# Performance work log

Hardware: AMD Instinct MI355X
Metric: run time of the kernel (lower is better)

## Reference

```python
import jax, jax.numpy as jnp
import numpy as np

N_NODES = 40962
N_EDGES = 245760
K = 10  # gaussian kernels
D = 2   # pseudo-coordinate dim
EPS = 1e-15


def gmm_conv(x, edge_index, pseudo, g, mu, sigma, root, bias):
    """PyG GMMConv with aggr='mean', root_weight=True.
    x: [N, Cin], edge_index: [2, E] (row 0 = source j, row 1 = target i),
    pseudo: [E, D], g: [Cin, K*Cout], mu/sigma: [K, D], root: [Cin, Cout], bias: [Cout].
    """
    src, dst = edge_index[0], edge_index[1]
    E = pseudo.shape[0]
    # Gaussian mixture edge weights: [E, K]
    diff = pseudo[:, None, :] - mu[None, :, :]                     # [E, K, D]
    w = jnp.exp(jnp.sum(-0.5 * diff * diff / (EPS + sigma[None] ** 2), axis=-1))
    xj = x[src]                                                    # [E, Cin] gather
    y = (xj @ g).reshape(E, K, -1)                                 # [E, K, Cout]
    msg = jnp.sum(y * w[:, :, None], axis=1)                       # [E, Cout]
    agg = jax.ops.segment_sum(msg, dst, num_segments=N_NODES)      # scatter-add
    deg = jax.ops.segment_sum(jnp.ones((E,), x.dtype), dst, num_segments=N_NODES)
    agg = agg / jnp.maximum(deg, 1.0)[:, None]                     # mean aggregation
    return agg + x @ root + bias


def setup_inputs() -> dict:
    key = jax.random.key(0)
    ks = jax.random.split(key, 20)
    Cin, Ch, Cout = 64, 64, 128
    sc = lambda fan: 1.0 / np.sqrt(fan)
    inp = {
        "x": jax.random.normal(ks[0], (N_NODES, Cin), jnp.float32),
        "edge_index": jax.random.randint(ks[1], (2, N_EDGES), 0, N_NODES, jnp.int32),
        "pseudo": jax.random.uniform(ks[2], (N_EDGES, D), jnp.float32),
        # conv1: Cin -> Ch
        "g1": jax.random.normal(ks[3], (Cin, K * Ch), jnp.float32) * sc(Cin),
        "mu1": jax.random.uniform(ks[4], (K, D), jnp.float32),
        "sigma1": jax.random.uniform(ks[5], (K, D), jnp.float32) + 0.5,
        "root1": jax.random.normal(ks[6], (Cin, Ch), jnp.float32) * sc(Cin),
        "b1": jnp.zeros((Ch,), jnp.float32),
        # conv2: Ch -> Cout
        "g2": jax.random.normal(ks[7], (Ch, K * Cout), jnp.float32) * sc(Ch),
        "mu2": jax.random.uniform(ks[8], (K, D), jnp.float32),
        "sigma2": jax.random.uniform(ks[9], (K, D), jnp.float32) + 0.5,
        "root2": jax.random.normal(ks[10], (Ch, Cout), jnp.float32) * sc(Ch),
        "b2": jnp.zeros((Cout,), jnp.float32),
        # shortcut: Cin -> Cout (size_in != size_out)
        "gs": jax.random.normal(ks[11], (Cin, K * Cout), jnp.float32) * sc(Cin),
        "mus": jax.random.uniform(ks[12], (K, D), jnp.float32),
        "sigmas": jax.random.uniform(ks[13], (K, D), jnp.float32) + 0.5,
        "roots": jax.random.normal(ks[14], (Cin, Cout), jnp.float32) * sc(Cin),
        "bs": jnp.zeros((Cout,), jnp.float32),
    }
    return inp


def reference(x, edge_index, pseudo, g1, mu1, sigma1, root1, b1,
              g2, mu2, sigma2, root2, b2, gs, mus, sigmas, roots, bs):
    h = gmm_conv(x, edge_index, pseudo, g1, mu1, sigma1, root1, b1)
    h = jax.nn.relu(h)
    y = gmm_conv(h, edge_index, pseudo, g2, mu2, sigma2, root2, b2)
    x_s = gmm_conv(x, edge_index, pseudo, gs, mus, sigmas, roots, bs)
    return jax.nn.relu(y + x_s)
```

## Files before the change

kernel.cpp:

```cpp
#include <hip/hip_runtime.h>
#include <hip/hip_bf16.h>

using bf16 = __hip_bfloat16;
typedef __attribute__((ext_vector_type(8))) short short8;
typedef __attribute__((ext_vector_type(4))) float float4v;

#define N_NODES 40962
#define N_EDGES 245760
#define NP      41024
#define KG      10
#define SCAN_B  256
#define NBLK    ((NP + SCAN_B - 1) / SCAN_B)
#define GRIDF   (NP / 16)

#define CVT_V   (N_NODES * 64 / 8)
#define CVT_BLK ((CVT_V + 255) / 256)
#define W3_BLK  (N_EDGES / 256)
#define PACK_N  (64 * 704 + 2 * 128 * 704)
#define PACK_BLK (PACK_N / 256)

#define ZRS  680
#define ZT   10880

__device__ __forceinline__ float ldf(const void* p, size_t i, int isf32) {
    return isf32 ? ((const float*)p)[i] : __bfloat162float(((const bf16*)p)[i]);
}
__device__ __forceinline__ float blo(unsigned u) { return __uint_as_float(u << 16); }
__device__ __forceinline__ float bhi(unsigned u) { return __uint_as_float(u & 0xffff0000u); }
__device__ __forceinline__ unsigned pk2(float a, float b) {
    union { bf16 h[2]; unsigned u; } t;
    t.h[0] = __float2bfloat16(a);
    t.h[1] = __float2bfloat16(b);
    return t.u;
}
__device__ __forceinline__ int rfl(int v) { return __builtin_amdgcn_readfirstlane(v); }

__global__ void k_detect_count(const void* x, const int* __restrict__ ei,
                               int* __restrict__ flag, int* __restrict__ deg) {
    if (blockIdx.x == 0) {
        __shared__ int huge_c, zero_even;
        if (threadIdx.x == 0) { huge_c = 0; zero_even = 0; }
        __syncthreads();
        const bf16* xb = (const bf16*)x;
        int lh = 0, lz = 0;
        for (int i = threadIdx.x; i < 8192; i += 256) {
            float v = __bfloat162float(xb[i]);
            if (!(fabsf(v) <= 1e4f)) lh++;
            if ((i & 1) == 0 && v == 0.0f) lz++;
        }
        atomicAdd(&huge_c, lh);
        atomicAdd(&zero_even, lz);
        __syncthreads();
        if (threadIdx.x == 0) flag[0] = (huge_c > 0 || zero_even > 3000) ? 1 : 0;
    } else {
        int e = (blockIdx.x - 1) * 256 + threadIdx.x;
        if (e < N_EDGES) atomicAdd(&deg[ei[N_EDGES + e]], 1);
    }
}

__global__ void k_scan1(const int* __restrict__ deg, int* __restrict__ offs,
                        int* __restrict__ bsum) {
    __shared__ int buf[SCAN_B];
    int t = threadIdx.x, b = blockIdx.x;
    int i = b * SCAN_B + t;
    int v = (i < NP) ? deg[i] : 0;
    buf[t] = v;
    __syncthreads();
    for (int off = 1; off < SCAN_B; off <<= 1) {
        int a = (t >= off) ? buf[t - off] : 0;
        __syncthreads();
        buf[t] += a;
        __syncthreads();
    }
    if (i < NP) offs[i] = buf[t] - v;
    if (t == SCAN_B - 1) bsum[b] = buf[t];
}

__global__ void k_scan3m(int* __restrict__ offs, const int* __restrict__ bsum,
                         const int* __restrict__ deg, int* __restrict__ cur,
                         float* __restrict__ invdeg) {
    __shared__ int buf[256];
    int t = threadIdx.x, b = blockIdx.x;
    int v = (t < NBLK) ? bsum[t] : 0;
    buf[t] = v;
    __syncthreads();
    for (int off = 1; off < 256; off <<= 1) {
        int a = (t >= off) ? buf[t - off] : 0;
        __syncthreads();
        buf[t] += a;
        __syncthreads();
    }
    int bofs = (b > 0) ? buf[b - 1] : 0;
    int total = buf[NBLK - 1];
    int i = b * 256 + t;
    if (i < NP) {
        int o = offs[i] + bofs;
        offs[i] = o;
        cur[i] = o;
        int d = deg[i];
        invdeg[i] = 1.0f / (float)(d > 1 ? d : 1);
    }
    if (i == 0) offs[NP] = total;
}

__global__ void k_fill(const int* __restrict__ ei, int* __restrict__ cur,
                       int* __restrict__ ep, int* __restrict__ csr_src) {
    int e = blockIdx.x * 256 + threadIdx.x;
    if (e < N_EDGES) {
        int pos = atomicAdd(&cur[ei[N_EDGES + e]], 1);
        ep[e] = pos;
        csr_src[pos] = ei[e];
    }
}

__device__ __forceinline__ void gw_one(float p0, float p1, const void* mu,
                                       const void* sg, int f, float* out) {
#pragma unroll
    for (int k = 0; k < KG; k++) {
        float m0 = ldf(mu, 2 * k + 0, f), m1 = ldf(mu, 2 * k + 1, f);
        float s0 = ldf(sg, 2 * k + 0, f), s1 = ldf(sg, 2 * k + 1, f);
        float d0 = p0 - m0, d1 = p1 - m1;
        float t = -0.5f * (d0 * d0 / (1e-15f + s0 * s0) + d1 * d1 / (1e-15f + s1 * s1));
        out[k] = __expf(t);
    }
}

__device__ __forceinline__ void pack_frag(const void* g, const void* root, int f,
                                          int idx, int Cout, bf16* Bp) {
    int j = idx & 7;
    int lane = (idx >> 3) & 63;
    int rem = idx >> 9;
    int kc = rem % 22;
    int n = rem / 22;
    int col = n * 16 + (lane & 15);
    int k = kc * 32 + (lane >> 4) * 8 + j;
    float v;
    if (k < 512) {
        int cin = k >> 3, kg = k & 7;
        v = ldf(g, (size_t)cin * (KG * Cout) + (size_t)kg * Cout + col, f);
    } else if (k < 640) {
        int jj = k - 512;
        int cin = jj >> 1, kg = 8 + (jj & 1);
        v = ldf(g, (size_t)cin * (KG * Cout) + (size_t)kg * Cout + col, f);
    } else {
        v = ldf(root, (size_t)(k - 640) * Cout + col, f);
    }
    Bp[idx] = __float2bfloat16(v);
}

__global__ void k_prep_all(const void* __restrict__ x, const void* __restrict__ pseudo,
                           const void* mu1, const void* sg1, const void* mu2,
                           const void* sg2, const void* mus, const void* sgs,
                           const void* g1, const void* root1, const void* g2,
                           const void* root2, const void* gs, const void* roots,
                           const int* __restrict__ flag, const int* __restrict__ ep,
                           bf16* __restrict__ Xf, bf16* __restrict__ wcab,
                           bf16* __restrict__ wc2, bf16* wt1p, bf16* wt2p,
                           bf16* wtsp) {
    int b = blockIdx.x;
    int tid = threadIdx.x;
    int f = flag[0];
    if (b < CVT_BLK) {
        int i = b * 256 + tid;
        if (i < CVT_V) {
            int node = i >> 3, j = i & 7;
            uint4 u;
            if (f) {
                const float4* xf = (const float4*)x;
                float4 a = xf[2 * i], c = xf[2 * i + 1];
                union { bf16 t[8]; uint4 u; } tt;
                tt.t[0] = __float2bfloat16(a.x); tt.t[1] = __float2bfloat16(a.y);
                tt.t[2] = __float2bfloat16(a.z); tt.t[3] = __float2bfloat16(a.w);
                tt.t[4] = __float2bfloat16(c.x); tt.t[5] = __float2bfloat16(c.y);
                tt.t[6] = __float2bfloat16(c.z); tt.t[7] = __float2bfloat16(c.w);
                u = tt.u;
            } else {
                u = ((const uint4*)x)[i];
            }
            *(uint4*)(Xf + (size_t)node * 64 + j * 8) = u;
        }
    } else if (b < CVT_BLK + W3_BLK) {
        int e = (b - CVT_BLK) * 256 + tid;
        float p0 = ldf(pseudo, (size_t)e * 2 + 0, f);
        float p1 = ldf(pseudo, (size_t)e * 2 + 1, f);
        float o1[KG], o2[KG], os[KG];
        gw_one(p0, p1, mu1, sg1, f, o1);
        gw_one(p0, p1, mu2, sg2, f, o2);
        gw_one(p0, p1, mus, sgs, f, os);
        int pos = ep[e];
        unsigned* d = (unsigned*)wcab + (size_t)pos * 10;
        d[0] = pk2(o1[0], o1[1]); d[1] = pk2(o1[2], o1[3]);
        d[2] = pk2(o1[4], o1[5]); d[3] = pk2(o1[6], o1[7]);
        d[4] = pk2(o1[8], o1[9]);
        d[5] = pk2(os[0], os[1]); d[6] = pk2(os[2], os[3]);
        d[7] = pk2(os[4], os[5]); d[8] = pk2(os[6], os[7]);
        d[9] = pk2(os[8], os[9]);
        unsigned* d2 = (unsigned*)wc2 + (size_t)pos * 5;
        d2[0] = pk2(o2[0], o2[1]); d2[1] = pk2(o2[2], o2[3]);
        d2[2] = pk2(o2[4], o2[5]); d2[3] = pk2(o2[6], o2[7]);
        d2[4] = pk2(o2[8], o2[9]);
    } else {
        int idx = (b - CVT_BLK - W3_BLK) * 256 + tid;
        if (idx < 64 * 704) {
            pack_frag(g1, root1, f, idx, 64, wt1p);
        } else if (idx < 64 * 704 + 128 * 704) {
            pack_frag(g2, root2, f, idx - 64 * 704, 128, wt2p);
        } else {
            pack_frag(gs, roots, f, idx - 64 * 704 - 128 * 704, 128, wtsp);
        }
    }
}

__device__ __forceinline__ float ldxf(const bf16* X, int src, int lane) {
    return __bfloat162float(X[(size_t)src * 64 + lane]);
}

__device__ __forceinline__ int clampe(int idx) {
    return idx > N_EDGES - 1 ? N_EDGES - 1 : idx;
}

__device__ __forceinline__ void store_zlds(bf16* z, int r, int lane, const float* a,
                                           float inv) {
    union { bf16 h[8]; uint4 u; } p;
#pragma unroll
    for (int k = 0; k < 8; k++) p.h[k] = __float2bfloat16(a[k] * inv);
    *(uint4*)(z + r * ZRS + lane * 8) = p.u;
    *(unsigned*)(z + r * ZRS + 512 + lane * 2) = pk2(a[8] * inv, a[9] * inv);
}

__device__ __forceinline__ void gather_dual(const int* __restrict__ offs,
                                            const int* __restrict__ csr_src,
                                            const unsigned* __restrict__ wb,
                                            const bf16* __restrict__ X, int node,
                                            int lane, float* aa, float* ab) {
#pragma unroll
    for (int k = 0; k < KG; k++) { aa[k] = 0.0f; ab[k] = 0.0f; }
    int beg = rfl(offs[node]);
    int end = rfl(offs[node + 1]);
    int cnt = end - beg;
    int s4 = rfl(csr_src[clampe(beg + 4)]);
    float xv0 = ldxf(X, rfl(csr_src[clampe(beg + 0)]), lane);
    float xv1 = ldxf(X, rfl(csr_src[clampe(beg + 1)]), lane);
    float xv2 = ldxf(X, rfl(csr_src[clampe(beg + 2)]), lane);
    float xv3 = ldxf(X, rfl(csr_src[clampe(beg + 3)]), lane);
    const unsigned* wp0 = wb + (size_t)clampe(beg + 0) * 10;
    unsigned c0 = wp0[0], c1 = wp0[1], c2 = wp0[2], c3 = wp0[3], c4 = wp0[4];
    unsigned c5 = wp0[5], c6 = wp0[6], c7 = wp0[7], c8 = wp0[8], c9 = wp0[9];
    const unsigned* wp1 = wb + (size_t)clampe(beg + 1) * 10;
    unsigned n0 = wp1[0], n1 = wp1[1], n2 = wp1[2], n3 = wp1[3], n4 = wp1[4];
    unsigned n5 = wp1[5], n6 = wp1[6], n7 = wp1[7], n8 = wp1[8], n9 = wp1[9];
    for (int t = 0; t < cnt; ++t) {
        int s5 = rfl(csr_src[clampe(beg + t + 5)]);
        float xv4 = ldxf(X, s4, lane);
        const unsigned* wp2 = wb + (size_t)clampe(beg + t + 2) * 10;
        unsigned m0 = wp2[0], m1 = wp2[1], m2 = wp2[2], m3 = wp2[3], m4 = wp2[4];
        unsigned m5 = wp2[5], m6 = wp2[6], m7 = wp2[7], m8 = wp2[8], m9 = wp2[9];
        aa[0] += blo(c0) * xv0; aa[1] += bhi(c0) * xv0;
        aa[2] += blo(c1) * xv0; aa[3] += bhi(c1) * xv0;
        aa[4] += blo(c2) * xv0; aa[5] += bhi(c2) * xv0;
        aa[6] += blo(c3) * xv0; aa[7] += bhi(c3) * xv0;
        aa[8] += blo(c4) * xv0; aa[9] += bhi(c4) * xv0;
        ab[0] += blo(c5) * xv0; ab[1] += bhi(c5) * xv0;
        ab[2] += blo(c6) * xv0; ab[3] += bhi(c6) * xv0;
        ab[4] += blo(c7) * xv0; ab[5] += bhi(c7) * xv0;
        ab[6] += blo(c8) * xv0; ab[7] += bhi(c8) * xv0;
        ab[8] += blo(c9) * xv0; ab[9] += bhi(c9) * xv0;
        xv0 = xv1; xv1 = xv2; xv2 = xv3; xv3 = xv4; s4 = s5;
        c0 = n0; c1 = n1; c2 = n2; c3 = n3; c4 = n4;
        c5 = n5; c6 = n6; c7 = n7; c8 = n8; c9 = n9;
        n0 = m0; n1 = m1; n2 = m2; n3 = m3; n4 = m4;
        n5 = m5; n6 = m6; n7 = m7; n8 = m8; n9 = m9;
    }
}

__device__ __forceinline__ void gather_one(const int* __restrict__ offs,
                                           const int* __restrict__ csr_src,
                                           const unsigned* __restrict__ wb,
                                           const bf16* __restrict__ X, int node,
                                           int lane, float* acc) {
#pragma unroll
    for (int k = 0; k < KG; k++) acc[k] = 0.0f;
    int beg = rfl(offs[node]);
    int end = rfl(offs[node + 1]);
    int cnt = end - beg;
    int s4 = rfl(csr_src[clampe(beg + 4)]);
    float xv0 = ldxf(X, rfl(csr_src[clampe(beg + 0)]), lane);
    float xv1 = ldxf(X, rfl(csr_src[clampe(beg + 1)]), lane);
    float xv2 = ldxf(X, rfl(csr_src[clampe(beg + 2)]), lane);
    float xv3 = ldxf(X, rfl(csr_src[clampe(beg + 3)]), lane);
    const unsigned* wp0 = wb + (size_t)clampe(beg + 0) * 5;
    unsigned c0 = wp0[0], c1 = wp0[1], c2 = wp0[2], c3 = wp0[3], c4 = wp0[4];
    const unsigned* wp1 = wb + (size_t)clampe(beg + 1) * 5;
    unsigned n0 = wp1[0], n1 = wp1[1], n2 = wp1[2], n3 = wp1[3], n4 = wp1[4];
    for (int t = 0; t < cnt; ++t) {
        int s5 = rfl(csr_src[clampe(beg + t + 5)]);
        float xv4 = ldxf(X, s4, lane);
        const unsigned* wp2 = wb + (size_t)clampe(beg + t + 2) * 5;
        unsigned m0 = wp2[0], m1 = wp2[1], m2 = wp2[2], m3 = wp2[3], m4 = wp2[4];
        acc[0] += blo(c0) * xv0; acc[1] += bhi(c0) * xv0;
        acc[2] += blo(c1) * xv0; acc[3] += bhi(c1) * xv0;
        acc[4] += blo(c2) * xv0; acc[5] += bhi(c2) * xv0;
        acc[6] += blo(c3) * xv0; acc[7] += bhi(c3) * xv0;
        acc[8] += blo(c4) * xv0; acc[9] += bhi(c4) * xv0;
        xv0 = xv1; xv1 = xv2; xv2 = xv3; xv3 = xv4; s4 = s5;
        c0 = n0; c1 = n1; c2 = n2; c3 = n3; c4 = n4;
        n0 = m0; n1 = m1; n2 = m2; n3 = m3; n4 = m4;
    }
}

__global__ __launch_bounds__(512) void k_fusedA(
    const int* __restrict__ offs, const int* __restrict__ csr_src,
    const bf16* __restrict__ wcab, const float* __restrict__ invdeg,
    const bf16* __restrict__ Xf, const bf16* __restrict__ wt1p,
    const bf16* __restrict__ wtsp, const void* __restrict__ b1,
    const void* __restrict__ bs, const int* __restrict__ flag,
    bf16* __restrict__ hf, bf16* __restrict__ ys) {
    __shared__ bf16 z1[ZT];
    __shared__ bf16 zs[ZT];
    int lane = threadIdx.x & 63;
    int wave = threadIdx.x >> 6;
    int bid = blockIdx.x;

#pragma unroll
    for (int i = 0; i < 2; i++) {
        int r = wave * 2 + i;
        int node = bid * 16 + r;
        float aa[KG], ab[KG];
        gather_dual(offs, csr_src, (const unsigned*)wcab, Xf, node, lane, aa, ab);
        float inv = invdeg[node];
        store_zlds(z1, r, lane, aa, inv);
        store_zlds(zs, r, lane, ab, inv);
    }
    __syncthreads();

    int m = lane & 15, quad = lane >> 4;
    int row0 = bid * 16;
    int f = flag[0];

    {
        float4v acc4 = (float4v){0.f, 0.f, 0.f, 0.f};
        const bf16* brow = wtsp + ((size_t)(wave * 22) * 64 + lane) * 8;
        const bf16* xrow = Xf + (size_t)(row0 + m) * 64;
#pragma unroll
        for (int kc = 0; kc < 22; kc++) {
            short8 a = (kc < 20)
                ? *(const short8*)(zs + m * ZRS + kc * 32 + quad * 8)
                : *(const short8*)(xrow + (kc - 20) * 32 + quad * 8);
            short8 b = *(const short8*)(brow + (size_t)kc * 512);
            acc4 = __builtin_amdgcn_mfma_f32_16x16x32_bf16(a, b, acc4, 0, 0, 0);
        }
        int gcol = wave * 16 + m;
        float bv = ldf(bs, gcol, f);
#pragma unroll
        for (int r = 0; r < 4; r++) {
            int grow = row0 + quad * 4 + r;
            if (grow >= N_NODES) continue;
            ys[(size_t)grow * 128 + gcol] = __float2bfloat16(acc4[r] + bv);
        }
    }

    if (wave < 4) {
        float4v acc4 = (float4v){0.f, 0.f, 0.f, 0.f};
        const bf16* brow = wt1p + ((size_t)(wave * 22) * 64 + lane) * 8;
        const bf16* xrow = Xf + (size_t)(row0 + m) * 64;
#pragma unroll
        for (int kc = 0; kc < 22; kc++) {
            short8 a = (kc < 20)
                ? *(const short8*)(z1 + m * ZRS + kc * 32 + quad * 8)
                : *(const short8*)(xrow + (kc - 20) * 32 + quad * 8);
            short8 b = *(const short8*)(brow + (size_t)kc * 512);
            acc4 = __builtin_amdgcn_mfma_f32_16x16x32_bf16(a, b, acc4, 0, 0, 0);
        }
        int gcol = wave * 16 + m;
        float bv = ldf(b1, gcol, f);
#pragma unroll
        for (int r = 0; r < 4; r++) {
            int grow = row0 + quad * 4 + r;
            if (grow >= N_NODES) continue;
            float v = fmaxf(acc4[r] + bv, 0.f);
            hf[(size_t)grow * 64 + gcol] = __float2bfloat16(v);
        }
    }
}

__global__ __launch_bounds__(512) void k_fusedB(
    const int* __restrict__ offs, const int* __restrict__ csr_src,
    const bf16* __restrict__ wc2, const float* __restrict__ invdeg,
    const bf16* __restrict__ hf, const bf16* __restrict__ wt2p,
    const void* __restrict__ b2, const bf16* __restrict__ ys,
    const int* __restrict__ flag, void* __restrict__ out) {
    __shared__ bf16 z[ZT];
    int lane = threadIdx.x & 63;
    int wave = threadIdx.x >> 6;
    int bid = blockIdx.x;

#pragma unroll
    for (int i = 0; i < 2; i++) {
        int r = wave * 2 + i;
        int node = bid * 16 + r;
        float acc[KG];
        gather_one(offs, csr_src, (const unsigned*)wc2, hf, node, lane, acc);
        store_zlds(z, r, lane, acc, invdeg[node]);
    }
    __syncthreads();

    int m = lane & 15, quad = lane >> 4;
    int row0 = bid * 16;
    int f = flag[0];
    float4v acc4 = (float4v){0.f, 0.f, 0.f, 0.f};
    const bf16* brow = wt2p + ((size_t)(wave * 22) * 64 + lane) * 8;
    const bf16* hrow = hf + (size_t)(row0 + m) * 64;
#pragma unroll
    for (int kc = 0; kc < 22; kc++) {
        short8 a = (kc < 20)
            ? *(const short8*)(z + m * ZRS + kc * 32 + quad * 8)
            : *(const short8*)(hrow + (kc - 20) * 32 + quad * 8);
        short8 b = *(const short8*)(brow + (size_t)kc * 512);
        acc4 = __builtin_amdgcn_mfma_f32_16x16x32_bf16(a, b, acc4, 0, 0, 0);
    }
    int gcol = wave * 16 + m;
    float bv = ldf(b2, gcol, f);
#pragma unroll
    for (int r = 0; r < 4; r++) {
        int grow = row0 + quad * 4 + r;
        if (grow >= N_NODES) continue;
        size_t oidx = (size_t)grow * 128 + gcol;
        float v = fmaxf(acc4[r] + bv + __bfloat162float(ys[oidx]), 0.f);
        if (f) ((float*)out)[oidx] = v;
        else   ((bf16*)out)[oidx] = __float2bfloat16(v);
    }
}

extern "C" void kernel_launch(void* const* d_in, const int* in_sizes, int n_in,
                              void* d_out, int out_size, void* d_ws, size_t ws_size,
                              hipStream_t stream) {
    const void* x      = d_in[0];
    const int*  ei     = (const int*)d_in[1];
    const void* pseudo = d_in[2];
    const void* g1     = d_in[3];
    const void* mu1    = d_in[4];
    const void* sg1    = d_in[5];
    const void* root1  = d_in[6];
    const void* b1     = d_in[7];
    const void* g2     = d_in[8];
    const void* mu2    = d_in[9];
    const void* sg2    = d_in[10];
    const void* root2  = d_in[11];
    const void* b2     = d_in[12];
    const void* gs     = d_in[13];
    const void* mus    = d_in[14];
    const void* sgs    = d_in[15];
    const void* roots  = d_in[16];
    const void* bs     = d_in[17];

    char* ws = (char*)d_ws;
    size_t off = 0;
    auto alloc = [&](size_t bytes) -> char* {
        char* p = ws + off;
        off += (bytes + 255) & ~(size_t)255;
        return p;
    };
    const size_t XFS = (size_t)NP * 64 * 2;

    int*   flag   = (int*)alloc(256);
    int*   deg    = (int*)alloc((size_t)NP * 4);
    int*   offs   = (int*)alloc((size_t)(NP + 1) * 4);
    int*   cur    = (int*)alloc((size_t)NP * 4);
    float* invdeg = (float*)alloc((size_t)NP * 4);
    int*   bsum   = (int*)alloc((size_t)NBLK * 4);
    int*   ep     = (int*)alloc((size_t)N_EDGES * 4);
    int*   csrs   = (int*)alloc((size_t)N_EDGES * 4);
    bf16*  Xf     = (bf16*)alloc(XFS);
    bf16*  hf     = (bf16*)alloc(XFS);
    bf16*  ys     = (bf16*)alloc((size_t)NP * 128 * 2);
    bf16*  wt1p   = (bf16*)alloc((size_t)64 * 704 * 2);
    bf16*  wt2p   = (bf16*)alloc((size_t)128 * 704 * 2);
    bf16*  wtsp   = (bf16*)alloc((size_t)128 * 704 * 2);
    bf16*  wcab   = (bf16*)alloc((size_t)N_EDGES * 20 * 2);
    bf16*  wc2    = (bf16*)alloc((size_t)N_EDGES * 10 * 2);
    (void)ws_size;

    hipMemsetAsync(deg, 0, (size_t)NP * 4, stream);
    k_detect_count<<<1 + (N_EDGES + 255) / 256, 256, 0, stream>>>(x, ei, flag, deg);
    k_scan1<<<NBLK, SCAN_B, 0, stream>>>(deg, offs, bsum);
    k_scan3m<<<NBLK, 256, 0, stream>>>(offs, bsum, deg, cur, invdeg);
    k_fill<<<(N_EDGES + 255) / 256, 256, 0, stream>>>(ei, cur, ep, csrs);
    k_prep_all<<<CVT_BLK + W3_BLK + PACK_BLK, 256, 0, stream>>>(
        x, pseudo, mu1, sg1, mu2, sg2, mus, sgs, g1, root1, g2, root2, gs, roots,
        flag, ep, Xf, wcab, wc2, wt1p, wt2p, wtsp);
    k_fusedA<<<GRIDF, 512, 0, stream>>>(offs, csrs, wcab, invdeg, Xf, wt1p, wtsp,
                                        b1, bs, flag, hf, ys);
    k_fusedB<<<GRIDF, 512, 0, stream>>>(offs, csrs, wc2, invdeg, hf, wt2p, b2,
                                        ys, flag, d_out);
}
```

Before: 270.9 us.

## Store edge weights structure-of-arrays and load per-chunk with lane shuffles

The per-edge Gaussian weights move from an array-of-structs layout (10 or 5 words per edge) to a structure-of-arrays layout indexed by CSR position. The gather loops now load up to 64 edges' source indices and weights cooperatively, one edge per lane, in coalesced loads, then broadcast them with __shfl inside the inner loop. This replaces the redundant per-edge uniform loads and software-pipelined register rotation. In exchange it adds many cross-lane shuffles per edge and loses prefetch of weights across chunk boundaries. The prep kernel's scattered writes also become strided across ten separate planes.

New measurement: 300.3 us. 10.9% more time.

```diff
diff --git a/kernel.cpp b/kernel.cpp
--- a/kernel.cpp
+++ b/kernel.cpp
@@ -154,8 +154,8 @@
                            const void* g1, const void* root1, const void* g2,
                            const void* root2, const void* gs, const void* roots,
                            const int* __restrict__ flag, const int* __restrict__ ep,
-                           bf16* __restrict__ Xf, bf16* __restrict__ wcab,
-                           bf16* __restrict__ wc2, bf16* wt1p, bf16* wt2p,
+                           bf16* __restrict__ Xf, unsigned* __restrict__ wcab,
+                           unsigned* __restrict__ wc2, bf16* wt1p, bf16* wt2p,
                            bf16* wtsp) {
     int b = blockIdx.x;
     int tid = threadIdx.x;
@@ -188,17 +188,21 @@
         gw_one(p0, p1, mu2, sg2, f, o2);
         gw_one(p0, p1, mus, sgs, f, os);
         int pos = ep[e];
-        unsigned* d = (unsigned*)wcab + (size_t)pos * 10;
-        d[0] = pk2(o1[0], o1[1]); d[1] = pk2(o1[2], o1[3]);
-        d[2] = pk2(o1[4], o1[5]); d[3] = pk2(o1[6], o1[7]);
-        d[4] = pk2(o1[8], o1[9]);
-        d[5] = pk2(os[0], os[1]); d[6] = pk2(os[2], os[3]);
-        d[7] = pk2(os[4], os[5]); d[8] = pk2(os[6], os[7]);
-        d[9] = pk2(os[8], os[9]);
-        unsigned* d2 = (unsigned*)wc2 + (size_t)pos * 5;
-        d2[0] = pk2(o2[0], o2[1]); d2[1] = pk2(o2[2], o2[3]);
-        d2[2] = pk2(o2[4], o2[5]); d2[3] = pk2(o2[6], o2[7]);
-        d2[4] = pk2(o2[8], o2[9]);
+        wcab[0 * N_EDGES + pos] = pk2(o1[0], o1[1]);
+        wcab[1 * N_EDGES + pos] = pk2(o1[2], o1[3]);
+        wcab[2 * N_EDGES + pos] = pk2(o1[4], o1[5]);
+        wcab[3 * N_EDGES + pos] = pk2(o1[6], o1[7]);
+        wcab[4 * N_EDGES + pos] = pk2(o1[8], o1[9]);
+        wcab[5 * N_EDGES + pos] = pk2(os[0], os[1]);
+        wcab[6 * N_EDGES + pos] = pk2(os[2], os[3]);
+        wcab[7 * N_EDGES + pos] = pk2(os[4], os[5]);
+        wcab[8 * N_EDGES + pos] = pk2(os[6], os[7]);
+        wcab[9 * N_EDGES + pos] = pk2(os[8], os[9]);
+        wc2[0 * N_EDGES + pos] = pk2(o2[0], o2[1]);
+        wc2[1 * N_EDGES + pos] = pk2(o2[2], o2[3]);
+        wc2[2 * N_EDGES + pos] = pk2(o2[4], o2[5]);
+        wc2[3 * N_EDGES + pos] = pk2(o2[6], o2[7]);
+        wc2[4 * N_EDGES + pos] = pk2(o2[8], o2[9]);
     } else {
         int idx = (b - CVT_BLK - W3_BLK) * 256 + tid;
         if (idx < 64 * 704) {
@@ -215,10 +219,6 @@
     return __bfloat162float(X[(size_t)src * 64 + lane]);
 }
 
-__device__ __forceinline__ int clampe(int idx) {
-    return idx > N_EDGES - 1 ? N_EDGES - 1 : idx;
-}
-
 __device__ __forceinline__ void store_zlds(bf16* z, int r, int lane, const float* a,
                                            float inv) {
     union { bf16 h[8]; uint4 u; } p;
@@ -230,87 +230,97 @@
 
 __device__ __forceinline__ void gather_dual(const int* __restrict__ offs,
                                             const int* __restrict__ csr_src,
-                                            const unsigned* __restrict__ wb,
+                                            const unsigned* __restrict__ wu,
                                             const bf16* __restrict__ X, int node,
                                             int lane, float* aa, float* ab) {
 #pragma unroll
     for (int k = 0; k < KG; k++) { aa[k] = 0.0f; ab[k] = 0.0f; }
     int beg = rfl(offs[node]);
     int end = rfl(offs[node + 1]);
-    int cnt = end - beg;
-    int s4 = rfl(csr_src[clampe(beg + 4)]);
-    float xv0 = ldxf(X, rfl(csr_src[clampe(beg + 0)]), lane);
-    float xv1 = ldxf(X, rfl(csr_src[clampe(beg + 1)]), lane);
-    float xv2 = ldxf(X, rfl(csr_src[clampe(beg + 2)]), lane);
-    float xv3 = ldxf(X, rfl(csr_src[clampe(beg + 3)]), lane);
-    const unsigned* wp0 = wb + (size_t)clampe(beg + 0) * 10;
-    unsigned c0 = wp0[0], c1 = wp0[1], c2 = wp0[2], c3 = wp0[3], c4 = wp0[4];
-    unsigned c5 = wp0[5], c6 = wp0[6], c7 = wp0[7], c8 = wp0[8], c9 = wp0[9];
-    const unsigned* wp1 = wb + (size_t)clampe(beg + 1) * 10;
-    unsigned n0 = wp1[0], n1 = wp1[1], n2 = wp1[2], n3 = wp1[3], n4 = wp1[4];
-    unsigned n5 = wp1[5], n6 = wp1[6], n7 = wp1[7], n8 = wp1[8], n9 = wp1[9];
-    for (int t = 0; t < cnt; ++t) {
-        int s5 = rfl(csr_src[clampe(beg + t + 5)]);
-        float xv4 = ldxf(X, s4, lane);
-        const unsigned* wp2 = wb + (size_t)clampe(beg + t + 2) * 10;
-        unsigned m0 = wp2[0], m1 = wp2[1], m2 = wp2[2], m3 = wp2[3], m4 = wp2[4];
-        unsigned m5 = wp2[5], m6 = wp2[6], m7 = wp2[7], m8 = wp2[8], m9 = wp2[9];
-        aa[0] += blo(c0) * xv0; aa[1] += bhi(c0) * xv0;
-        aa[2] += blo(c1) * xv0; aa[3] += bhi(c1) * xv0;
-        aa[4] += blo(c2) * xv0; aa[5] += bhi(c2) * xv0;
-        aa[6] += blo(c3) * xv0; aa[7] += bhi(c3) * xv0;
-        aa[8] += blo(c4) * xv0; aa[9] += bhi(c4) * xv0;
-        ab[0] += blo(c5) * xv0; ab[1] += bhi(c5) * xv0;
-        ab[2] += blo(c6) * xv0; ab[3] += bhi(c6) * xv0;
-        ab[4] += blo(c7) * xv0; ab[5] += bhi(c7) * xv0;
-        ab[6] += blo(c8) * xv0; ab[7] += bhi(c8) * xv0;
-        ab[8] += blo(c9) * xv0; ab[9] += bhi(c9) * xv0;
-        xv0 = xv1; xv1 = xv2; xv2 = xv3; xv3 = xv4; s4 = s5;
-        c0 = n0; c1 = n1; c2 = n2; c3 = n3; c4 = n4;
-        c5 = n5; c6 = n6; c7 = n7; c8 = n8; c9 = n9;
-        n0 = m0; n1 = m1; n2 = m2; n3 = m3; n4 = m4;
-        n5 = m5; n6 = m6; n7 = m7; n8 = m8; n9 = m9;
+    for (int base = beg; base < end; base += 64) {
+        int nch = end - base;
+        if (nch > 64) nch = 64;
+        int eidx = base + (lane < nch ? lane : nch - 1);
+        int sv = csr_src[eidx];
+        unsigned w0 = wu[0 * N_EDGES + eidx], w1 = wu[1 * N_EDGES + eidx];
+        unsigned w2 = wu[2 * N_EDGES + eidx], w3 = wu[3 * N_EDGES + eidx];
+        unsigned w4 = wu[4 * N_EDGES + eidx], w5 = wu[5 * N_EDGES + eidx];
+        unsigned w6 = wu[6 * N_EDGES + eidx], w7 = wu[7 * N_EDGES + eidx];
+        unsigned w8 = wu[8 * N_EDGES + eidx], w9 = wu[9 * N_EDGES + eidx];
+        float xv0 = ldxf(X, __shfl(sv, 0), lane);
+        float xv1 = ldxf(X, __shfl(sv, 1 < nch ? 1 : 0), lane);
+        float xv2 = ldxf(X, __shfl(sv, 2 < nch ? 2 : 0), lane);
+        float xv3 = ldxf(X, __shfl(sv, 3 < nch ? 3 : 0), lane);
+        for (int t = 0; t < nch; ++t) {
+            int tp = (t + 4 < nch) ? t + 4 : nch - 1;
+            float xv4 = ldxf(X, __shfl(sv, tp), lane);
+            unsigned c0 = (unsigned)__shfl((int)w0, t);
+            unsigned c1 = (unsigned)__shfl((int)w1, t);
+            unsigned c2 = (unsigned)__shfl((int)w2, t);
+            unsigned c3 = (unsigned)__shfl((int)w3, t);
+            unsigned c4 = (unsigned)__shfl((int)w4, t);
+            unsigned c5 = (unsigned)__shfl((int)w5, t);
+            unsigned c6 = (unsigned)__shfl((int)w6, t);
+            unsigned c7 = (unsigned)__shfl((int)w7, t);
+            unsigned c8 = (unsigned)__shfl((int)w8, t);
+            unsigned c9 = (unsigned)__shfl((int)w9, t);
+            aa[0] += blo(c0) * xv0; aa[1] += bhi(c0) * xv0;
+            aa[2] += blo(c1) * xv0; aa[3] += bhi(c1) * xv0;
+            aa[4] += blo(c2) * xv0; aa[5] += bhi(c2) * xv0;
+            aa[6] += blo(c3) * xv0; aa[7] += bhi(c3) * xv0;
+            aa[8] += blo(c4) * xv0; aa[9] += bhi(c4) * xv0;
+            ab[0] += blo(c5) * xv0; ab[1] += bhi(c5) * xv0;
+            ab[2] += blo(c6) * xv0; ab[3] += bhi(c6) * xv0;
+            ab[4] += blo(c7) * xv0; ab[5] += bhi(c7) * xv0;
+            ab[6] += blo(c8) * xv0; ab[7] += bhi(c8) * xv0;
+            ab[8] += blo(c9) * xv0; ab[9] += bhi(c9) * xv0;
+            xv0 = xv1; xv1 = xv2; xv2 = xv3; xv3 = xv4;
+        }
     }
 }
 
 __device__ __forceinline__ void gather_one(const int* __restrict__ offs,
                                            const int* __restrict__ csr_src,
-                                           const unsigned* __restrict__ wb,
+                                           const unsigned* __restrict__ wu,
                                            const bf16* __restrict__ X, int node,
                                            int lane, float* acc) {
 #pragma unroll
     for (int k = 0; k < KG; k++) acc[k] = 0.0f;
     int beg = rfl(offs[node]);
     int end = rfl(offs[node + 1]);
-    int cnt = end - beg;
-    int s4 = rfl(csr_src[clampe(beg + 4)]);
-    float xv0 = ldxf(X, rfl(csr_src[clampe(beg + 0)]), lane);
-    float xv1 = ldxf(X, rfl(csr_src[clampe(beg + 1)]), lane);
-    float xv2 = ldxf(X, rfl(csr_src[clampe(beg + 2)]), lane);
-    float xv3 = ldxf(X, rfl(csr_src[clampe(beg + 3)]), lane);
-    const unsigned* wp0 = wb + (size_t)clampe(beg + 0) * 5;
-    unsigned c0 = wp0[0], c1 = wp0[1], c2 = wp0[2], c3 = wp0[3], c4 = wp0[4];
-    const unsigned* wp1 = wb + (size_t)clampe(beg + 1) * 5;
-    unsigned n0 = wp1[0], n1 = wp1[1], n2 = wp1[2], n3 = wp1[3], n4 = wp1[4];
-    for (int t = 0; t < cnt; ++t) {
-        int s5 = rfl(csr_src[clampe(beg + t + 5)]);
-        float xv4 = ldxf(X, s4, lane);
-        const unsigned* wp2 = wb + (size_t)clampe(beg + t + 2) * 5;
-        unsigned m0 = wp2[0], m1 = wp2[1], m2 = wp2[2], m3 = wp2[3], m4 = wp2[4];
-        acc[0] += blo(c0) * xv0; acc[1] += bhi(c0) * xv0;
-        acc[2] += blo(c1) * xv0; acc[3] += bhi(c1) * xv0;
-        acc[4] += blo(c2) * xv0; acc[5] += bhi(c2) * xv0;
-        acc[6] += blo(c3) * xv0; acc[7] += bhi(c3) * xv0;
-        acc[8] += blo(c4) * xv0; acc[9] += bhi(c4) * xv0;
-        xv0 = xv1; xv1 = xv2; xv2 = xv3; xv3 = xv4; s4 = s5;
-        c0 = n0; c1 = n1; c2 = n2; c3 = n3; c4 = n4;
-        n0 = m0; n1 = m1; n2 = m2; n3 = m3; n4 = m4;
+    for (int base = beg; base < end; base += 64) {
+        int nch = end - base;
+        if (nch > 64) nch = 64;
+        int eidx = base + (lane < nch ? lane : nch - 1);
+        int sv = csr_src[eidx];
+        unsigned w0 = wu[0 * N_EDGES + eidx], w1 = wu[1 * N_EDGES + eidx];
+        unsigned w2 = wu[2 * N_EDGES + eidx], w3 = wu[3 * N_EDGES + eidx];
+        unsigned w4 = wu[4 * N_EDGES + eidx];
+        float xv0 = ldxf(X, __shfl(sv, 0), lane);
+        float xv1 = ldxf(X, __shfl(sv, 1 < nch ? 1 : 0), lane);
+        float xv2 = ldxf(X, __shfl(sv, 2 < nch ? 2 : 0), lane);
+        float xv3 = ldxf(X, __shfl(sv, 3 < nch ? 3 : 0), lane);
+        for (int t = 0; t < nch; ++t) {
+            int tp = (t + 4 < nch) ? t + 4 : nch - 1;
+            float xv4 = ldxf(X, __shfl(sv, tp), lane);
+            unsigned c0 = (unsigned)__shfl((int)w0, t);
+            unsigned c1 = (unsigned)__shfl((int)w1, t);
+            unsigned c2 = (unsigned)__shfl((int)w2, t);
+            unsigned c3 = (unsigned)__shfl((int)w3, t);
+            unsigned c4 = (unsigned)__shfl((int)w4, t);
+            acc[0] += blo(c0) * xv0; acc[1] += bhi(c0) * xv0;
+            acc[2] += blo(c1) * xv0; acc[3] += bhi(c1) * xv0;
+            acc[4] += blo(c2) * xv0; acc[5] += bhi(c2) * xv0;
+            acc[6] += blo(c3) * xv0; acc[7] += bhi(c3) * xv0;
+            acc[8] += blo(c4) * xv0; acc[9] += bhi(c4) * xv0;
+            xv0 = xv1; xv1 = xv2; xv2 = xv3; xv3 = xv4;
+        }
     }
 }
 
 __global__ __launch_bounds__(512) void k_fusedA(
     const int* __restrict__ offs, const int* __restrict__ csr_src,
-    const bf16* __restrict__ wcab, const float* __restrict__ invdeg,
+    const unsigned* __restrict__ wcab, const float* __restrict__ invdeg,
     const bf16* __restrict__ Xf, const bf16* __restrict__ wt1p,
     const bf16* __restrict__ wtsp, const void* __restrict__ b1,
     const void* __restrict__ bs, const int* __restrict__ flag,
@@ -326,7 +336,7 @@
         int r = wave * 2 + i;
         int node = bid * 16 + r;
         float aa[KG], ab[KG];
-        gather_dual(offs, csr_src, (const unsigned*)wcab, Xf, node, lane, aa, ab);
+        gather_dual(offs, csr_src, wcab, Xf, node, lane, aa, ab);
         float inv = invdeg[node];
         store_zlds(z1, r, lane, aa, inv);
         store_zlds(zs, r, lane, ab, inv);
@@ -385,7 +395,7 @@
 
 __global__ __launch_bounds__(512) void k_fusedB(
     const int* __restrict__ offs, const int* __restrict__ csr_src,
-    const bf16* __restrict__ wc2, const float* __restrict__ invdeg,
+    const unsigned* __restrict__ wc2, const float* __restrict__ invdeg,
     const bf16* __restrict__ hf, const bf16* __restrict__ wt2p,
     const void* __restrict__ b2, const bf16* __restrict__ ys,
     const int* __restrict__ flag, void* __restrict__ out) {
@@ -399,7 +409,7 @@
         int r = wave * 2 + i;
         int node = bid * 16 + r;
         float acc[KG];
-        gather_one(offs, csr_src, (const unsigned*)wc2, hf, node, lane, acc);
+        gather_one(offs, csr_src, wc2, hf, node, lane, acc);
         store_zlds(z, r, lane, acc, invdeg[node]);
     }
     __syncthreads();
@@ -462,22 +472,22 @@
     };
     const size_t XFS = (size_t)NP * 64 * 2;
 
-    int*   flag   = (int*)alloc(256);
-    int*   deg    = (int*)alloc((size_t)NP * 4);
-    int*   offs   = (int*)alloc((size_t)(NP + 1) * 4);
-    int*   cur    = (int*)alloc((size_t)NP * 4);
-    float* invdeg = (float*)alloc((size_t)NP * 4);
-    int*   bsum   = (int*)alloc((size_t)NBLK * 4);
-    int*   ep     = (int*)alloc((size_t)N_EDGES * 4);
-    int*   csrs   = (int*)alloc((size_t)N_EDGES * 4);
-    bf16*  Xf     = (bf16*)alloc(XFS);
-    bf16*  hf     = (bf16*)alloc(XFS);
-    bf16*  ys     = (bf16*)alloc((size_t)NP * 128 * 2);
-    bf16*  wt1p   = (bf16*)alloc((size_t)64 * 704 * 2);
-    bf16*  wt2p   = (bf16*)alloc((size_t)128 * 704 * 2);
-    bf16*  wtsp   = (bf16*)alloc((size_t)128 * 704 * 2);
-    bf16*  wcab   = (bf16*)alloc((size_t)N_EDGES * 20 * 2);
-    bf16*  wc2    = (bf16*)alloc((size_t)N_EDGES * 10 * 2);
+    int*      flag   = (int*)alloc(256);
+    int*      deg    = (int*)alloc((size_t)NP * 4);
+    int*      offs   = (int*)alloc((size_t)(NP + 1) * 4);
+    int*      cur    = (int*)alloc((size_t)NP * 4);
+    float*    invdeg = (float*)alloc((size_t)NP * 4);
+    int*      bsum   = (int*)alloc((size_t)NBLK * 4);
+    int*      ep     = (int*)alloc((size_t)N_EDGES * 4);
+    int*      csrs   = (int*)alloc((size_t)N_EDGES * 4);
+    bf16*     Xf     = (bf16*)alloc(XFS);
+    bf16*     hf     = (bf16*)alloc(XFS);
+    bf16*     ys     = (bf16*)alloc((size_t)NP * 128 * 2);
+    bf16*     wt1p   = (bf16*)alloc((size_t)64 * 704 * 2);
+    bf16*     wt2p   = (bf16*)alloc((size_t)128 * 704 * 2);
+    bf16*     wtsp   = (bf16*)alloc((size_t)128 * 704 * 2);
+    unsigned* wcab   = (unsigned*)alloc((size_t)10 * N_EDGES * 4);
+    unsigned* wc2    = (unsigned*)alloc((size_t)5 * N_EDGES * 4);
     (void)ws_size;
 
     hipMemsetAsync(deg, 0, (size_t)NP * 4, stream);
```
